# Kernel tuning notes

Hardware: AMD Instinct MI355X
Metric: run time of the kernel (lower is better)

Reference implementation:

```python
import jax, jax.numpy as jnp
import numpy as np

N_HEADS = 16
NEG = -1000000000.0  # masked_fill value from the original code


def setup_inputs() -> dict:
    key = jax.random.key(0)
    ks = jax.random.split(key, 7)
    D = 1024
    x = jax.random.normal(ks[0], (2, 2048, D), dtype=jnp.float32)
    s = 1.0 / np.sqrt(D)
    Wq = jax.random.normal(ks[1], (D, D), dtype=jnp.float32) * s
    bq = jax.random.normal(ks[2], (D,), dtype=jnp.float32) * 0.01
    Wk = jax.random.normal(ks[3], (D, D), dtype=jnp.float32) * s
    bk = jax.random.normal(ks[4], (D,), dtype=jnp.float32) * 0.01
    Wv = jax.random.normal(ks[5], (D, D), dtype=jnp.float32) * s
    bv = jax.random.normal(ks[6], (D,), dtype=jnp.float32) * 0.01
    return {"x": x, "Wq": Wq, "bq": bq, "Wk": Wk, "bk": bk, "Wv": Wv, "bv": bv}


def reference(x, Wq, bq, Wk, bk, Wv, bv):
    B, S, D = x.shape
    H = N_HEADS
    dh = D // H
    # nn.Linear: x @ W.T + b
    Q = (x @ Wq.T + bq).reshape(B, S, H, dh)
    K = (x @ Wk.T + bk).reshape(B, S, H, dh)
    V = (x @ Wv.T + bv).reshape(B, S, H, dh)
    # NOTE: original scales by sqrt(n_heads), not sqrt(d_head) -- faithful.
    scale = jnp.asarray(H, x.dtype) ** 0.5
    scores = jnp.einsum('bqhd,bkhd->bhqk', Q, K) / scale  # [B,H,S,S]
    # Original: mask = triu(ones, diag=1); scores.masked_fill(mask == 0, -1e9)
    # i.e. positions where the STRICT-UPPER mask is False (lower triangle incl.
    # diagonal) get -1e9. Faithful reproduction of that (buggy) behavior.
    triu = jnp.triu(jnp.ones((S, S), dtype=bool), k=1)  # [S,S]
    scores = jnp.where(triu[None, None, :, :], scores, jnp.asarray(NEG, x.dtype))
    probs = jax.nn.softmax(scores, axis=-1)
    # dropout is identity at inference
    out = jnp.einsum('bhqk,bkhd->bqhd', probs, V).reshape(B, S, D)
    return out
```

## Files before the change

kernel.cpp:

```cpp
#include <hip/hip_runtime.h>
#include <stdint.h>

typedef unsigned short u16;
typedef __attribute__((ext_vector_type(8))) short bf16x8;
typedef __attribute__((ext_vector_type(4))) float floatx4;

#define MFMA16(a, b, c) __builtin_amdgcn_mfma_f32_16x16x32_bf16(a, b, c, 0, 0, 0)
#define MEMFENCE asm volatile("" ::: "memory")

#if __has_builtin(__builtin_amdgcn_exp2f)
#define EXP2(x) __builtin_amdgcn_exp2f(x)
#else
#define EXP2(x) __expf(0.6931471805599453f * (x))
#endif

__device__ __forceinline__ u16 f2bf(float f) {
  unsigned u = __builtin_bit_cast(unsigned, f);
  return (u16)((u + 0x7FFFu + ((u >> 16) & 1u)) >> 16);
}
__device__ __forceinline__ u16 f2bf_hu(float f) {
  return (u16)((__builtin_bit_cast(unsigned, f) + 0x8000u) >> 16);
}
__device__ __forceinline__ float bf2f(u16 v) {
  return __builtin_bit_cast(float, (unsigned)v << 16);
}

__device__ __forceinline__ void glds16(void* lds, const void* g) {
  __builtin_amdgcn_global_load_lds((const __attribute__((address_space(1))) void*)g,
                                   (__attribute__((address_space(3))) void*)lds,
                                   16, 0, 0);
}

__global__ __launch_bounds__(256) void cvt_all(
    const float* __restrict__ x, const float* __restrict__ w0,
    const float* __restrict__ w1, const float* __restrict__ w2,
    u16* __restrict__ xb, u16* __restrict__ Wb) {
  const int bid = blockIdx.x;
  const float* src;
  u16* dst;
  int i;
  if (bid < 4096) {
    src = x; dst = xb; i = bid * 256 + threadIdx.x;
  } else {
    const int z = (bid - 4096) >> 10;
    src = (z == 0) ? w0 : (z == 1) ? w1 : w2;
    dst = Wb + (size_t)z * (1024 * 1024);
    i = ((bid - 4096) & 1023) * 256 + threadIdx.x;
  }
  float4 f = reinterpret_cast<const float4*>(src)[i];
  ushort4 o;
  o.x = f2bf(f.x); o.y = f2bf(f.y); o.z = f2bf(f.z); o.w = f2bf(f.w);
  reinterpret_cast<ushort4*>(dst)[i] = o;
}

__global__ __launch_bounds__(256, 3) void qkv_gemm(
    const u16* __restrict__ xb, const u16* __restrict__ Wb,
    const float* __restrict__ bq, const float* __restrict__ bk,
    const float* __restrict__ bv,
    u16* __restrict__ Qb, u16* __restrict__ Kb, u16* __restrict__ VTb) {
  __shared__ __attribute__((aligned(16))) u16 smem[2 * 128 * 64];
  u16* As = smem;
  u16* Bs = smem + 128 * 64;

  const int tid = threadIdx.x;
  const int w = tid >> 6, lane = tid & 63;
  const int lo = lane & 15, quad = lane >> 4;
  const int which = blockIdx.z;
  const int m0 = blockIdx.x * 128, n0 = blockIdx.y * 128;

  const u16* W = Wb + (size_t)which * (1024 * 1024);
  const int wm = (w >> 1) * 64, wn = (w & 1) * 64;

  floatx4 acc[4][4];
  for (int i = 0; i < 4; ++i)
    for (int j = 0; j < 4; ++j) acc[i][j] = (floatx4)0.f;

  const int arow = lane >> 3;
  const int aswz = ((lane & 7) ^ arow) * 8;

  for (int kt = 0; kt < 16; ++kt) {
    const int k0 = kt * 64;
    for (int j = 0; j < 4; ++j) {
      const int seg = w * 4 + j;
      glds16(As + seg * 512, xb + (size_t)(m0 + seg * 8 + arow) * 1024 + k0 + aswz);
      glds16(Bs + seg * 512, W + (size_t)(n0 + seg * 8 + arow) * 1024 + k0 + aswz);
    }
    __syncthreads();
    for (int kk = 0; kk < 2; ++kk) {
      const int swz = ((kk * 4 + quad) ^ (lo & 7)) * 8;
      bf16x8 af[4], bfr[4];
      for (int it = 0; it < 4; ++it)
        af[it] = *reinterpret_cast<const bf16x8*>(As + (wm + it * 16 + lo) * 64 + swz);
      for (int jt = 0; jt < 4; ++jt)
        bfr[jt] = *reinterpret_cast<const bf16x8*>(Bs + (wn + jt * 16 + lo) * 64 + swz);
      for (int it = 0; it < 4; ++it)
        for (int jt = 0; jt < 4; ++jt)
          acc[it][jt] = MFMA16(af[it], bfr[jt], acc[it][jt]);
    }
    __syncthreads();
  }

  const float* bias = (which == 0) ? bq : (which == 1) ? bk : bv;
  float bb[4];
  for (int jt = 0; jt < 4; ++jt) bb[jt] = bias[n0 + wn + jt * 16 + lo];
  const int b = m0 >> 11;

  if (which < 2) {
    const float scl = (which == 0) ? 0.36067376022224085f : 1.0f;
    u16* Tw = smem + w * (16 * 72);
    const int hblk = (n0 + wn) >> 6;
    u16* dst = ((which == 0) ? Qb : Kb) +
               ((size_t)(b * 16 + hblk) * 2048 + ((m0 & 2047) + wm)) * 64;
    for (int it = 0; it < 4; ++it) {
      for (int jt = 0; jt < 4; ++jt)
        for (int r = 0; r < 4; ++r) {
          const int m = quad * 4 + r, col = jt * 16 + lo;
          Tw[m * 72 + (((col >> 3) ^ (m & 7)) * 8) + (col & 7)] =
              f2bf((acc[it][jt][r] + bb[jt]) * scl);
        }
      MEMFENCE;
      for (int rd = 0; rd < 2; ++rd) {
        const int sr = rd * 8 + (lane >> 3), d8 = lane & 7;
        bf16x8 v = *reinterpret_cast<const bf16x8*>(Tw + sr * 72 + ((d8 ^ (sr & 7)) * 8));
        *reinterpret_cast<bf16x8*>(dst + (size_t)(it * 16 + sr) * 64 + d8 * 8) = v;
      }
      MEMFENCE;
    }
  } else {
    for (int pass = 0; pass < 2; ++pass) {
      if ((wm >> 6) == pass) {
        for (int it = 0; it < 4; ++it)
          for (int jt = 0; jt < 4; ++jt)
            for (int r = 0; r < 4; ++r) {
              const int n = wn + jt * 16 + lo;
              const int m = it * 16 + quad * 4 + r;
              smem[n * 72 + (((m >> 3) ^ (n & 7)) * 8) + (m & 7)] =
                  f2bf(acc[it][jt][r] + bb[jt]);
            }
      }
      __syncthreads();
      for (int rd = 0; rd < 4; ++rd) {
        const int n = (tid >> 3) + rd * 32, m8 = tid & 7;
        bf16x8 v = *reinterpret_cast<const bf16x8*>(smem + n * 72 + ((m8 ^ (n & 7)) * 8));
        const int ng = n0 + n, h = ng >> 6, d = ng & 63;
        const int s = (m0 & 2047) + pass * 64 + m8 * 8;
        *reinterpret_cast<bf16x8*>(VTb + ((size_t)(b * 16 + h) * 64 + d) * 2048 + s) = v;
      }
      __syncthreads();
    }
  }
}

__global__ __launch_bounds__(256, 3) void attn(
    const u16* __restrict__ Qb, const u16* __restrict__ Kb,
    const u16* __restrict__ VTb, float* __restrict__ out) {
  __shared__ __attribute__((aligned(16))) u16 Ks[2][64 * 64];
  __shared__ __attribute__((aligned(16))) u16 Vs[2][64 * 64];
  __shared__ __attribute__((aligned(16))) u16 Pt[4][2][16 * 64];

  const int L = blockIdx.x;
  const int bh = L & 31;
  const int s5 = L >> 5;
  const int qs = (s5 < 8) ? s5 : 23 - s5;
  const int kstart = 2 * qs;

  const int tid = threadIdx.x, w = tid >> 6, lane = tid & 63;
  const int lo = lane & 15, quad = lane >> 4;

  const u16* Qh = Qb + (size_t)bh * (2048 * 64);
  const u16* Kh = Kb + (size_t)bh * (2048 * 64);
  const u16* Vh = VTb + (size_t)bh * (64 * 2048);

  int qrow[2];
  bf16x8 qf[2][2];
  for (int s = 0; s < 2; ++s) {
    qrow[s] = qs * 128 + w * 32 + s * 16 + lo;
    qf[s][0] = *reinterpret_cast<const bf16x8*>(Qh + (size_t)qrow[s] * 64 + quad * 8);
    qf[s][1] = *reinterpret_cast<const bf16x8*>(Qh + (size_t)qrow[s] * 64 + 32 + quad * 8);
  }

  float lrun[2] = {0.f, 0.f};
  floatx4 acc[2][4];
  for (int s = 0; s < 2; ++s)
    for (int dt = 0; dt < 4; ++dt) acc[s][dt] = (floatx4)0.f;

  const int srow8 = lane >> 3, sblk = lane & 7;
  const int sswz = (sblk ^ srow8) * 8;

  for (int j = 0; j < 2; ++j) {
    const int b8 = (w * 2 + j) * 8;
    glds16(&Ks[0][b8 * 64], Kh + (size_t)(kstart * 64 + b8 + srow8) * 64 + sswz);
    glds16(&Vs[0][b8 * 64], Vh + (size_t)(b8 + srow8) * 2048 + kstart * 64 + sswz);
  }
  __syncthreads();

  for (int kt = kstart; kt < 32; ++kt) {
    const int cur = (kt - kstart) & 1, nxt = cur ^ 1;
    if (kt < 31)
      for (int j = 0; j < 2; ++j) {
        const int b8 = (w * 2 + j) * 8;
        glds16(&Ks[nxt][b8 * 64], Kh + (size_t)((kt + 1) * 64 + b8 + srow8) * 64 + sswz);
        glds16(&Vs[nxt][b8 * 64], Vh + (size_t)(b8 + srow8) * 2048 + (kt + 1) * 64 + sswz);
      }
    const u16* ksb = Ks[cur];
    const u16* vsb = Vs[cur];

    const int d2 = kt - 2 * qs;
    const bool skip = (d2 == 0) && (w >= 2);
    const bool maskp = ((d2 == 0) && (w < 2)) || ((d2 == 1) && (w >= 2));

    if (!skip) {
      floatx4 sc[2][4];
      for (int s = 0; s < 2; ++s)
        for (int t = 0; t < 4; ++t) sc[s][t] = (floatx4)0.f;
      for (int kk = 0; kk < 2; ++kk) {
        const int swz = ((kk * 4 + quad) ^ (lo & 7)) * 8;
        for (int t = 0; t < 4; ++t) {
          bf16x8 ka = *reinterpret_cast<const bf16x8*>(ksb + (t * 16 + lo) * 64 + swz);
          sc[0][t] = MFMA16(ka, qf[0][kk], sc[0][t]);
          sc[1][t] = MFMA16(ka, qf[1][kk], sc[1][t]);
        }
      }

      for (int s = 0; s < 2; ++s) {
        u16* ptw = &Pt[w][s][0];
        for (int t = 0; t < 4; ++t) {
          float p0 = EXP2(sc[s][t][0]), p1 = EXP2(sc[s][t][1]);
          float p2 = EXP2(sc[s][t][2]), p3 = EXP2(sc[s][t][3]);
          if (maskp) {
            const int key = kt * 64 + t * 16 + quad * 4;
            p0 = (key + 0 > qrow[s]) ? p0 : 0.f;
            p1 = (key + 1 > qrow[s]) ? p1 : 0.f;
            p2 = (key + 2 > qrow[s]) ? p2 : 0.f;
            p3 = (key + 3 > qrow[s]) ? p3 : 0.f;
          }
          lrun[s] += (p0 + p1) + (p2 + p3);
          ushort4 pk;
          pk.x = f2bf_hu(p0); pk.y = f2bf_hu(p1);
          pk.z = f2bf_hu(p2); pk.w = f2bf_hu(p3);
          u16* pdst = ptw + lo * 64 +
                      (((2 * t + (quad >> 1)) ^ (lo & 7)) * 8) + (quad & 1) * 4;
          *reinterpret_cast<ushort4*>(pdst) = pk;
        }
      }
      MEMFENCE;

      for (int kk = 0; kk < 2; ++kk) {
        const int pswz = ((kk * 4 + quad) ^ (lo & 7)) * 8;
        bf16x8 pb0 = *reinterpret_cast<const bf16x8*>(&Pt[w][0][lo * 64] + pswz);
        bf16x8 pb1 = *reinterpret_cast<const bf16x8*>(&Pt[w][1][lo * 64] + pswz);
        for (int dt = 0; dt < 4; ++dt) {
          bf16x8 va = *reinterpret_cast<const bf16x8*>(
              vsb + (dt * 16 + lo) * 64 + pswz);
          acc[0][dt] = MFMA16(va, pb0, acc[0][dt]);
          acc[1][dt] = MFMA16(va, pb1, acc[1][dt]);
        }
      }
      MEMFENCE;
    }
    __syncthreads();
  }

  const int b = bh >> 4, hh = bh & 15;
  for (int s = 0; s < 2; ++s) {
    float l = lrun[s];
    l += __shfl_xor(l, 16);
    l += __shfl_xor(l, 32);
    if (l != 0.f) {
      const float rl = 1.f / l;
      float* op = out + ((size_t)(b * 2048 + qrow[s])) * 1024 + hh * 64 + quad * 4;
      for (int dt = 0; dt < 4; ++dt) {
        float4 o4;
        o4.x = acc[s][dt][0] * rl; o4.y = acc[s][dt][1] * rl;
        o4.z = acc[s][dt][2] * rl; o4.w = acc[s][dt][3] * rl;
        *reinterpret_cast<float4*>(op + dt * 16) = o4;
      }
    }
  }
}

__global__ __launch_bounds__(256) void fix2047(const u16* __restrict__ VTb,
                                               float* __restrict__ out) {
  const int bh = blockIdx.x;
  const u16* Vh = VTb + (size_t)bh * (64 * 2048);
  const int t = threadIdx.x;
  const int d = t >> 2, j = t & 3;
  float s = 0.f;
  const u16* row = Vh + (size_t)d * 2048 + j * 512;
  for (int i = 0; i < 64; ++i) {
    bf16x8 v = *reinterpret_cast<const bf16x8*>(row + i * 8);
    for (int e = 0; e < 8; ++e) s += bf2f((u16)v[e]);
  }
  s += __shfl_xor(s, 1);
  s += __shfl_xor(s, 2);
  if (j == 0) {
    const int b = bh >> 4, h = bh & 15;
    out[((size_t)(b * 2048 + 2047)) * 1024 + h * 64 + d] = s * (1.f / 2048.f);
  }
}

extern "C" void kernel_launch(void* const* d_in, const int* in_sizes, int n_in,
                              void* d_out, int out_size, void* d_ws, size_t ws_size,
                              hipStream_t stream) {
  const float* x  = (const float*)d_in[0];
  const float* Wq = (const float*)d_in[1];
  const float* bq = (const float*)d_in[2];
  const float* Wk = (const float*)d_in[3];
  const float* bk = (const float*)d_in[4];
  const float* Wv = (const float*)d_in[5];
  const float* bv = (const float*)d_in[6];
  float* out = (float*)d_out;

  char* ws = (char*)d_ws;
  u16* xb  = (u16*)(ws);
  u16* Wb  = (u16*)(ws + (8u << 20));
  u16* Qb  = (u16*)(ws + (14u << 20));
  u16* Kb  = (u16*)(ws + (22u << 20));
  u16* VTb = (u16*)(ws + (30u << 20));

  cvt_all<<<7168, 256, 0, stream>>>(x, Wq, Wk, Wv, xb, Wb);
  qkv_gemm<<<dim3(32, 8, 3), 256, 0, stream>>>(xb, Wb, bq, bk, bv, Qb, Kb, VTb);
  attn<<<dim3(512), 256, 0, stream>>>(Qb, Kb, VTb, out);
  fix2047<<<dim3(32), 256, 0, stream>>>(VTb, out);
}
```

Measured before the change: 158.9 us.

## Restructure attention into single-wave blocks each handling a balanced pair of query tiles

```diff
diff --git a/kernel.cpp b/kernel.cpp
--- a/kernel.cpp
+++ b/kernel.cpp
@@ -7,6 +7,8 @@
 
 #define MFMA16(a, b, c) __builtin_amdgcn_mfma_f32_16x16x32_bf16(a, b, c, 0, 0, 0)
 #define MEMFENCE asm volatile("" ::: "memory")
+#define WAIT_VM0 asm volatile("s_waitcnt vmcnt(0)" ::: "memory")
+#define WAIT_LGKM0 asm volatile("s_waitcnt lgkmcnt(0)" ::: "memory")
 
 #if __has_builtin(__builtin_amdgcn_exp2f)
 #define EXP2(x) __builtin_amdgcn_exp2f(x)
@@ -151,79 +153,77 @@
   }
 }
 
-__global__ __launch_bounds__(256, 3) void attn(
+__global__ __launch_bounds__(64, 2) void attn(
     const u16* __restrict__ Qb, const u16* __restrict__ Kb,
     const u16* __restrict__ VTb, float* __restrict__ out) {
-  __shared__ __attribute__((aligned(16))) u16 Ks[2][64 * 64];
-  __shared__ __attribute__((aligned(16))) u16 Vs[2][64 * 64];
-  __shared__ __attribute__((aligned(16))) u16 Pt[4][2][16 * 64];
+  __shared__ __attribute__((aligned(16))) u16 Ks[64 * 64];
+  __shared__ __attribute__((aligned(16))) u16 Vs[64 * 64];
+  __shared__ __attribute__((aligned(16))) u16 Pt[2][16 * 64];
 
   const int L = blockIdx.x;
   const int bh = L & 31;
-  const int s5 = L >> 5;
-  const int qs = (s5 < 8) ? s5 : 23 - s5;
-  const int kstart = 2 * qs;
-
-  const int tid = threadIdx.x, w = tid >> 6, lane = tid & 63;
+  const int qtA = L >> 5;
+
+  const int lane = threadIdx.x & 63;
   const int lo = lane & 15, quad = lane >> 4;
 
   const u16* Qh = Qb + (size_t)bh * (2048 * 64);
   const u16* Kh = Kb + (size_t)bh * (2048 * 64);
   const u16* Vh = VTb + (size_t)bh * (64 * 2048);
 
-  int qrow[2];
-  bf16x8 qf[2][2];
-  for (int s = 0; s < 2; ++s) {
-    qrow[s] = qs * 128 + w * 32 + s * 16 + lo;
-    qf[s][0] = *reinterpret_cast<const bf16x8*>(Qh + (size_t)qrow[s] * 64 + quad * 8);
-    qf[s][1] = *reinterpret_cast<const bf16x8*>(Qh + (size_t)qrow[s] * 64 + 32 + quad * 8);
-  }
-
-  float lrun[2] = {0.f, 0.f};
-  floatx4 acc[2][4];
-  for (int s = 0; s < 2; ++s)
-    for (int dt = 0; dt < 4; ++dt) acc[s][dt] = (floatx4)0.f;
-
   const int srow8 = lane >> 3, sblk = lane & 7;
   const int sswz = (sblk ^ srow8) * 8;
-
-  for (int j = 0; j < 2; ++j) {
-    const int b8 = (w * 2 + j) * 8;
-    glds16(&Ks[0][b8 * 64], Kh + (size_t)(kstart * 64 + b8 + srow8) * 64 + sswz);
-    glds16(&Vs[0][b8 * 64], Vh + (size_t)(b8 + srow8) * 2048 + kstart * 64 + sswz);
-  }
-  __syncthreads();
-
-  for (int kt = kstart; kt < 32; ++kt) {
-    const int cur = (kt - kstart) & 1, nxt = cur ^ 1;
-    if (kt < 31)
-      for (int j = 0; j < 2; ++j) {
-        const int b8 = (w * 2 + j) * 8;
-        glds16(&Ks[nxt][b8 * 64], Kh + (size_t)((kt + 1) * 64 + b8 + srow8) * 64 + sswz);
-        glds16(&Vs[nxt][b8 * 64], Vh + (size_t)(b8 + srow8) * 2048 + (kt + 1) * 64 + sswz);
-      }
-    const u16* ksb = Ks[cur];
-    const u16* vsb = Vs[cur];
-
-    const int d2 = kt - 2 * qs;
-    const bool skip = (d2 == 0) && (w >= 2);
-    const bool maskp = ((d2 == 0) && (w < 2)) || ((d2 == 1) && (w >= 2));
-
-    if (!skip) {
+  const int b = bh >> 4, hh = bh & 15;
+
+#define STAGE(kt)                                                             \
+  for (int j = 0; j < 8; ++j) {                                               \
+    glds16(&Ks[j * 512], Kh + (size_t)((kt) * 64 + j * 8 + srow8) * 64 + sswz); \
+    glds16(&Vs[j * 512], Vh + (size_t)(j * 8 + srow8) * 2048 + (kt) * 64 + sswz); \
+  }
+
+  { STAGE(qtA >> 1); }
+
+  for (int p = 0; p < 2; ++p) {
+    const int qtp = (p == 0) ? qtA : 63 - qtA;
+    const int kstart = qtp >> 1;
+    const int n = 32 - kstart;
+
+    int qrow[2];
+    bf16x8 qf[2][2];
+    for (int s = 0; s < 2; ++s) {
+      qrow[s] = qtp * 32 + s * 16 + lo;
+      qf[s][0] = *reinterpret_cast<const bf16x8*>(Qh + (size_t)qrow[s] * 64 + quad * 8);
+      qf[s][1] = *reinterpret_cast<const bf16x8*>(Qh + (size_t)qrow[s] * 64 + 32 + quad * 8);
+    }
+
+    float lrun[2] = {0.f, 0.f};
+    floatx4 acc[2][4];
+    for (int s = 0; s < 2; ++s)
+      for (int dt = 0; dt < 4; ++dt) acc[s][dt] = (floatx4)0.f;
+
+    for (int i = 0; i < n; ++i) {
+      const int kt = kstart + i;
+      WAIT_VM0;
+      MEMFENCE;
+
       floatx4 sc[2][4];
       for (int s = 0; s < 2; ++s)
         for (int t = 0; t < 4; ++t) sc[s][t] = (floatx4)0.f;
+      bf16x8 va[2][4];
       for (int kk = 0; kk < 2; ++kk) {
         const int swz = ((kk * 4 + quad) ^ (lo & 7)) * 8;
         for (int t = 0; t < 4; ++t) {
-          bf16x8 ka = *reinterpret_cast<const bf16x8*>(ksb + (t * 16 + lo) * 64 + swz);
+          bf16x8 ka = *reinterpret_cast<const bf16x8*>(Ks + (t * 16 + lo) * 64 + swz);
           sc[0][t] = MFMA16(ka, qf[0][kk], sc[0][t]);
           sc[1][t] = MFMA16(ka, qf[1][kk], sc[1][t]);
         }
-      }
-
+        for (int dt = 0; dt < 4; ++dt)
+          va[kk][dt] = *reinterpret_cast<const bf16x8*>(Vs + (dt * 16 + lo) * 64 + swz);
+      }
+
+      const bool maskp = (i == 0);
       for (int s = 0; s < 2; ++s) {
-        u16* ptw = &Pt[w][s][0];
+        u16* ptw = &Pt[s][0];
         for (int t = 0; t < 4; ++t) {
           float p0 = EXP2(sc[s][t][0]), p1 = EXP2(sc[s][t][1]);
           float p2 = EXP2(sc[s][t][2]), p3 = EXP2(sc[s][t][3]);
@@ -245,38 +245,42 @@
       }
       MEMFENCE;
 
+      bf16x8 pb[2][2];
       for (int kk = 0; kk < 2; ++kk) {
         const int pswz = ((kk * 4 + quad) ^ (lo & 7)) * 8;
-        bf16x8 pb0 = *reinterpret_cast<const bf16x8*>(&Pt[w][0][lo * 64] + pswz);
-        bf16x8 pb1 = *reinterpret_cast<const bf16x8*>(&Pt[w][1][lo * 64] + pswz);
+        pb[0][kk] = *reinterpret_cast<const bf16x8*>(&Pt[0][lo * 64] + pswz);
+        pb[1][kk] = *reinterpret_cast<const bf16x8*>(&Pt[1][lo * 64] + pswz);
+      }
+      WAIT_LGKM0;
+      MEMFENCE;
+
+      if (i + 1 < n) { STAGE(kt + 1); }
+      else if (p == 0) { STAGE((63 - qtA) >> 1); }
+
+      for (int kk = 0; kk < 2; ++kk)
         for (int dt = 0; dt < 4; ++dt) {
-          bf16x8 va = *reinterpret_cast<const bf16x8*>(
-              vsb + (dt * 16 + lo) * 64 + pswz);
-          acc[0][dt] = MFMA16(va, pb0, acc[0][dt]);
-          acc[1][dt] = MFMA16(va, pb1, acc[1][dt]);
-        }
-      }
-      MEMFENCE;
-    }
-    __syncthreads();
-  }
-
-  const int b = bh >> 4, hh = bh & 15;
-  for (int s = 0; s < 2; ++s) {
-    float l = lrun[s];
-    l += __shfl_xor(l, 16);
-    l += __shfl_xor(l, 32);
-    if (l != 0.f) {
-      const float rl = 1.f / l;
-      float* op = out + ((size_t)(b * 2048 + qrow[s])) * 1024 + hh * 64 + quad * 4;
-      for (int dt = 0; dt < 4; ++dt) {
-        float4 o4;
-        o4.x = acc[s][dt][0] * rl; o4.y = acc[s][dt][1] * rl;
-        o4.z = acc[s][dt][2] * rl; o4.w = acc[s][dt][3] * rl;
-        *reinterpret_cast<float4*>(op + dt * 16) = o4;
-      }
-    }
-  }
+          acc[0][dt] = MFMA16(va[kk][dt], pb[0][kk], acc[0][dt]);
+          acc[1][dt] = MFMA16(va[kk][dt], pb[1][kk], acc[1][dt]);
+        }
+    }
+
+    for (int s = 0; s < 2; ++s) {
+      float l = lrun[s];
+      l += __shfl_xor(l, 16);
+      l += __shfl_xor(l, 32);
+      if (l != 0.f) {
+        const float rl = 1.f / l;
+        float* op = out + ((size_t)(b * 2048 + qrow[s])) * 1024 + hh * 64 + quad * 4;
+        for (int dt = 0; dt < 4; ++dt) {
+          float4 o4;
+          o4.x = acc[s][dt][0] * rl; o4.y = acc[s][dt][1] * rl;
+          o4.z = acc[s][dt][2] * rl; o4.w = acc[s][dt][3] * rl;
+          *reinterpret_cast<float4*>(op + dt * 16) = o4;
+        }
+      }
+    }
+  }
+#undef STAGE
 }
 
 __global__ __launch_bounds__(256) void fix2047(const u16* __restrict__ VTb,
@@ -320,6 +324,6 @@
 
   cvt_all<<<7168, 256, 0, stream>>>(x, Wq, Wk, Wv, xb, Wb);
   qkv_gemm<<<dim3(32, 8, 3), 256, 0, stream>>>(xb, Wb, bq, bk, bv, Qb, Kb, VTb);
-  attn<<<dim3(512), 256, 0, stream>>>(Qb, Kb, VTb, out);
+  attn<<<dim3(1024), 64, 0, stream>>>(Qb, Kb, VTb, out);
   fix2047<<<dim3(32), 256, 0, stream>>>(VTb, out);
 }
```

After: 171.0 us. 1.08x slower.

## Switch attention to 32x32 MFMA with register-shuffled P, smaller blocks

Applied to the files above, without the earlier changes.

```diff
diff --git a/kernel.cpp b/kernel.cpp
--- a/kernel.cpp
+++ b/kernel.cpp
@@ -4,8 +4,11 @@
 typedef unsigned short u16;
 typedef __attribute__((ext_vector_type(8))) short bf16x8;
 typedef __attribute__((ext_vector_type(4))) float floatx4;
+typedef __attribute__((ext_vector_type(16))) float floatx16;
+typedef __attribute__((ext_vector_type(4))) unsigned uintx4;
 
 #define MFMA16(a, b, c) __builtin_amdgcn_mfma_f32_16x16x32_bf16(a, b, c, 0, 0, 0)
+#define MFMA32(a, b, c) __builtin_amdgcn_mfma_f32_32x32x16_bf16(a, b, c, 0, 0, 0)
 #define MEMFENCE asm volatile("" ::: "memory")
 
 #if __has_builtin(__builtin_amdgcn_exp2f)
@@ -18,8 +21,10 @@
   unsigned u = __builtin_bit_cast(unsigned, f);
   return (u16)((u + 0x7FFFu + ((u >> 16) & 1u)) >> 16);
 }
-__device__ __forceinline__ u16 f2bf_hu(float f) {
-  return (u16)((__builtin_bit_cast(unsigned, f) + 0x8000u) >> 16);
+__device__ __forceinline__ unsigned pkbf(float a, float b) {
+  unsigned ua = __builtin_bit_cast(unsigned, a);
+  unsigned ub = __builtin_bit_cast(unsigned, b);
+  return ((ua + 0x8000u) >> 16) | ((ub + 0x8000u) & 0xFFFF0000u);
 }
 __device__ __forceinline__ float bf2f(u16 v) {
   return __builtin_bit_cast(float, (unsigned)v << 16);
@@ -151,131 +156,137 @@
   }
 }
 
-__global__ __launch_bounds__(256, 3) void attn(
+__global__ __launch_bounds__(128, 2) void attn(
     const u16* __restrict__ Qb, const u16* __restrict__ Kb,
     const u16* __restrict__ VTb, float* __restrict__ out) {
   __shared__ __attribute__((aligned(16))) u16 Ks[2][64 * 64];
   __shared__ __attribute__((aligned(16))) u16 Vs[2][64 * 64];
-  __shared__ __attribute__((aligned(16))) u16 Pt[4][2][16 * 64];
 
   const int L = blockIdx.x;
   const int bh = L & 31;
-  const int s5 = L >> 5;
-  const int qs = (s5 < 8) ? s5 : 23 - s5;
-  const int kstart = 2 * qs;
-
-  const int tid = threadIdx.x, w = tid >> 6, lane = tid & 63;
-  const int lo = lane & 15, quad = lane >> 4;
+  const int qt = L >> 5;
+  const int kstart = qt, n = 32 - qt;
+
+  const int tid = threadIdx.x;
+  const int wq = tid >> 6, lane = tid & 63;
+  const int l31 = lane & 31, h = lane >> 5;
 
   const u16* Qh = Qb + (size_t)bh * (2048 * 64);
   const u16* Kh = Kb + (size_t)bh * (2048 * 64);
   const u16* Vh = VTb + (size_t)bh * (64 * 2048);
 
-  int qrow[2];
-  bf16x8 qf[2][2];
-  for (int s = 0; s < 2; ++s) {
-    qrow[s] = qs * 128 + w * 32 + s * 16 + lo;
-    qf[s][0] = *reinterpret_cast<const bf16x8*>(Qh + (size_t)qrow[s] * 64 + quad * 8);
-    qf[s][1] = *reinterpret_cast<const bf16x8*>(Qh + (size_t)qrow[s] * 64 + 32 + quad * 8);
-  }
-
-  float lrun[2] = {0.f, 0.f};
-  floatx4 acc[2][4];
-  for (int s = 0; s < 2; ++s)
-    for (int dt = 0; dt < 4; ++dt) acc[s][dt] = (floatx4)0.f;
+  const int qrow = qt * 64 + wq * 32 + l31;
+  bf16x8 qf[4];
+  for (int kk = 0; kk < 4; ++kk)
+    qf[kk] = *reinterpret_cast<const bf16x8*>(Qh + (size_t)qrow * 64 + kk * 16 + h * 8);
+
+  float lrun = 0.f;
+  floatx16 acc[2];
+  acc[0] = (floatx16)0.f;
+  acc[1] = (floatx16)0.f;
 
   const int srow8 = lane >> 3, sblk = lane & 7;
   const int sswz = (sblk ^ srow8) * 8;
 
-  for (int j = 0; j < 2; ++j) {
-    const int b8 = (w * 2 + j) * 8;
-    glds16(&Ks[0][b8 * 64], Kh + (size_t)(kstart * 64 + b8 + srow8) * 64 + sswz);
-    glds16(&Vs[0][b8 * 64], Vh + (size_t)(b8 + srow8) * 2048 + kstart * 64 + sswz);
-  }
+#define STAGE(buf, kt_)                                                       \
+  for (int j = 0; j < 4; ++j) {                                               \
+    const int r0 = wq * 32 + j * 8;                                           \
+    glds16(&Ks[buf][r0 * 64], Kh + (size_t)((kt_) * 64 + r0 + srow8) * 64 + sswz); \
+    glds16(&Vs[buf][r0 * 64], Vh + (size_t)(r0 + srow8) * 2048 + (kt_) * 64 + sswz); \
+  }
+
+  STAGE(0, kstart);
   __syncthreads();
 
   for (int kt = kstart; kt < 32; ++kt) {
     const int cur = (kt - kstart) & 1, nxt = cur ^ 1;
-    if (kt < 31)
-      for (int j = 0; j < 2; ++j) {
-        const int b8 = (w * 2 + j) * 8;
-        glds16(&Ks[nxt][b8 * 64], Kh + (size_t)((kt + 1) * 64 + b8 + srow8) * 64 + sswz);
-        glds16(&Vs[nxt][b8 * 64], Vh + (size_t)(b8 + srow8) * 2048 + (kt + 1) * 64 + sswz);
-      }
+    if (kt < 31) { STAGE(nxt, kt + 1); }
     const u16* ksb = Ks[cur];
     const u16* vsb = Vs[cur];
 
-    const int d2 = kt - 2 * qs;
-    const bool skip = (d2 == 0) && (w >= 2);
-    const bool maskp = ((d2 == 0) && (w < 2)) || ((d2 == 1) && (w >= 2));
-
-    if (!skip) {
-      floatx4 sc[2][4];
-      for (int s = 0; s < 2; ++s)
-        for (int t = 0; t < 4; ++t) sc[s][t] = (floatx4)0.f;
-      for (int kk = 0; kk < 2; ++kk) {
-        const int swz = ((kk * 4 + quad) ^ (lo & 7)) * 8;
-        for (int t = 0; t < 4; ++t) {
-          bf16x8 ka = *reinterpret_cast<const bf16x8*>(ksb + (t * 16 + lo) * 64 + swz);
-          sc[0][t] = MFMA16(ka, qf[0][kk], sc[0][t]);
-          sc[1][t] = MFMA16(ka, qf[1][kk], sc[1][t]);
+    floatx16 sc[2];
+    sc[0] = (floatx16)0.f;
+    sc[1] = (floatx16)0.f;
+    for (int kk = 0; kk < 4; ++kk) {
+      const int ch = kk * 2 + h;
+      for (int m = 0; m < 2; ++m) {
+        const int row = m * 32 + l31;
+        bf16x8 ka = *reinterpret_cast<const bf16x8*>(
+            ksb + row * 64 + ((ch ^ (row & 7)) * 8));
+        sc[m] = MFMA32(ka, qf[kk], sc[m]);
+      }
+    }
+
+    const bool maskp = (kt == kstart);
+    unsigned pw[2][8];
+#pragma unroll
+    for (int m = 0; m < 2; ++m)
+#pragma unroll
+      for (int g = 0; g < 4; ++g) {
+        float p0 = EXP2(sc[m][4 * g + 0]), p1 = EXP2(sc[m][4 * g + 1]);
+        float p2 = EXP2(sc[m][4 * g + 2]), p3 = EXP2(sc[m][4 * g + 3]);
+        if (maskp) {
+          const int keyb = kt * 64 + m * 32 + 8 * g + 4 * h;
+          p0 = (keyb + 0 > qrow) ? p0 : 0.f;
+          p1 = (keyb + 1 > qrow) ? p1 : 0.f;
+          p2 = (keyb + 2 > qrow) ? p2 : 0.f;
+          p3 = (keyb + 3 > qrow) ? p3 : 0.f;
         }
-      }
-
-      for (int s = 0; s < 2; ++s) {
-        u16* ptw = &Pt[w][s][0];
-        for (int t = 0; t < 4; ++t) {
-          float p0 = EXP2(sc[s][t][0]), p1 = EXP2(sc[s][t][1]);
-          float p2 = EXP2(sc[s][t][2]), p3 = EXP2(sc[s][t][3]);
-          if (maskp) {
-            const int key = kt * 64 + t * 16 + quad * 4;
-            p0 = (key + 0 > qrow[s]) ? p0 : 0.f;
-            p1 = (key + 1 > qrow[s]) ? p1 : 0.f;
-            p2 = (key + 2 > qrow[s]) ? p2 : 0.f;
-            p3 = (key + 3 > qrow[s]) ? p3 : 0.f;
-          }
-          lrun[s] += (p0 + p1) + (p2 + p3);
-          ushort4 pk;
-          pk.x = f2bf_hu(p0); pk.y = f2bf_hu(p1);
-          pk.z = f2bf_hu(p2); pk.w = f2bf_hu(p3);
-          u16* pdst = ptw + lo * 64 +
-                      (((2 * t + (quad >> 1)) ^ (lo & 7)) * 8) + (quad & 1) * 4;
-          *reinterpret_cast<ushort4*>(pdst) = pk;
+        lrun += (p0 + p1) + (p2 + p3);
+        pw[m][2 * g] = pkbf(p0, p1);
+        pw[m][2 * g + 1] = pkbf(p2, p3);
+      }
+
+    unsigned y[2][4];
+#pragma unroll
+    for (int m = 0; m < 2; ++m)
+#pragma unroll
+      for (int lh = 0; lh < 2; ++lh)
+#pragma unroll
+        for (int j = 0; j < 2; ++j) {
+          const unsigned s = h ? pw[m][4 * lh + j] : pw[m][4 * lh + 2 + j];
+          y[m][2 * lh + j] = __shfl_xor(s, 32);
         }
-      }
-      MEMFENCE;
-
-      for (int kk = 0; kk < 2; ++kk) {
-        const int pswz = ((kk * 4 + quad) ^ (lo & 7)) * 8;
-        bf16x8 pb0 = *reinterpret_cast<const bf16x8*>(&Pt[w][0][lo * 64] + pswz);
-        bf16x8 pb1 = *reinterpret_cast<const bf16x8*>(&Pt[w][1][lo * 64] + pswz);
-        for (int dt = 0; dt < 4; ++dt) {
-          bf16x8 va = *reinterpret_cast<const bf16x8*>(
-              vsb + (dt * 16 + lo) * 64 + pswz);
-          acc[0][dt] = MFMA16(va, pb0, acc[0][dt]);
-          acc[1][dt] = MFMA16(va, pb1, acc[1][dt]);
-        }
-      }
-      MEMFENCE;
+
+    bf16x8 pb[4];
+#pragma unroll
+    for (int c = 0; c < 4; ++c) {
+      const int m = c >> 1, lh = c & 1;
+      uintx4 u;
+      u.x = h ? y[m][2 * lh]      : pw[m][4 * lh];
+      u.y = h ? y[m][2 * lh + 1]  : pw[m][4 * lh + 1];
+      u.z = h ? pw[m][4 * lh + 2] : y[m][2 * lh];
+      u.w = h ? pw[m][4 * lh + 3] : y[m][2 * lh + 1];
+      pb[c] = __builtin_bit_cast(bf16x8, u);
+    }
+
+    for (int c = 0; c < 4; ++c) {
+      const int ch = c * 2 + h;
+      for (int dt = 0; dt < 2; ++dt) {
+        const int row = dt * 32 + l31;
+        bf16x8 va = *reinterpret_cast<const bf16x8*>(
+            vsb + row * 64 + ((ch ^ (row & 7)) * 8));
+        acc[dt] = MFMA32(va, pb[c], acc[dt]);
+      }
     }
     __syncthreads();
   }
-
-  const int b = bh >> 4, hh = bh & 15;
-  for (int s = 0; s < 2; ++s) {
-    float l = lrun[s];
-    l += __shfl_xor(l, 16);
-    l += __shfl_xor(l, 32);
-    if (l != 0.f) {
-      const float rl = 1.f / l;
-      float* op = out + ((size_t)(b * 2048 + qrow[s])) * 1024 + hh * 64 + quad * 4;
-      for (int dt = 0; dt < 4; ++dt) {
+#undef STAGE
+
+  lrun += __shfl_xor(lrun, 32);
+  if (lrun != 0.f) {
+    const float rl = 1.f / lrun;
+    const int b = bh >> 4, hh = bh & 15;
+    float* op = out + ((size_t)(b * 2048 + qrow)) * 1024 + hh * 64;
+    for (int dt = 0; dt < 2; ++dt)
+      for (int g = 0; g < 4; ++g) {
         float4 o4;
-        o4.x = acc[s][dt][0] * rl; o4.y = acc[s][dt][1] * rl;
-        o4.z = acc[s][dt][2] * rl; o4.w = acc[s][dt][3] * rl;
-        *reinterpret_cast<float4*>(op + dt * 16) = o4;
-      }
-    }
+        o4.x = acc[dt][4 * g + 0] * rl;
+        o4.y = acc[dt][4 * g + 1] * rl;
+        o4.z = acc[dt][4 * g + 2] * rl;
+        o4.w = acc[dt][4 * g + 3] * rl;
+        *reinterpret_cast<float4*>(op + dt * 32 + 8 * g + 4 * h) = o4;
+      }
   }
 }
 
@@ -320,6 +331,6 @@
 
   cvt_all<<<7168, 256, 0, stream>>>(x, Wq, Wk, Wv, xb, Wb);
   qkv_gemm<<<dim3(32, 8, 3), 256, 0, stream>>>(xb, Wb, bq, bk, bv, Qb, Kb, VTb);
-  attn<<<dim3(512), 256, 0, stream>>>(Qb, Kb, VTb, out);
+  attn<<<dim3(1024), 128, 0, stream>>>(Qb, Kb, VTb, out);
   fix2047<<<dim3(32), 256, 0, stream>>>(VTb, out);
 }
```

New measurement: 165.5 us. 1.04x slower.
